# Kernel tuning notes

Hardware: AMD Instinct MI355X
Metric: run time of the kernel (lower is better)

The kernel has to match this reference:

```python
import jax, jax.numpy as jnp
import numpy as np
from jax import lax

B, T, F, H = 8192, 512, 24, 12


def setup_inputs() -> dict:
    key = jax.random.key(0)
    ks = jax.random.split(key, 12)
    s_in = 1.0 / np.sqrt(H)  # PyTorch RNN init scale: U(-1/sqrt(H), 1/sqrt(H))
    u = lambda k, shape, s: jax.random.uniform(k, shape, jnp.float32, -s, s)
    return {
        "x": jax.random.normal(ks[0], (B, T, F), jnp.float32),
        "W_ih": u(ks[1], (H, F), s_in),
        "b_ih": u(ks[2], (H,), s_in),
        "W_hh": u(ks[3], (H, H), s_in),
        "b_hh": u(ks[4], (H,), s_in),
        "W1": u(ks[5], (H, H), 1.0 / np.sqrt(H)),
        "b1": u(ks[6], (H,), 1.0 / np.sqrt(H)),
        "W2": u(ks[7], (H, H), 1.0 / np.sqrt(H)),
        "b2": u(ks[8], (H,), 1.0 / np.sqrt(H)),
        "W3": u(ks[9], (1, H), 1.0 / np.sqrt(H)),
        "b3": u(ks[10], (1,), 1.0 / np.sqrt(H)),
    }


def reference(x, W_ih, b_ih, W_hh, b_hh, W1, b1, W2, b2, W3, b3):
    # Precompute input projection for all timesteps: [B,T,H]
    xp = jnp.einsum("btf,hf->bth", x, W_ih) + b_ih

    def step(h, xt):  # h: [B,H], xt: [B,H]
        h = jnp.tanh(xt + h @ W_hh.T + b_hh)
        return h, None

    h0 = jnp.zeros((x.shape[0], W_hh.shape[0]), x.dtype)
    hT, _ = lax.scan(step, h0, jnp.swapaxes(xp, 0, 1))  # scan over time

    out = jax.nn.relu(hT @ W1.T + b1)
    out = jax.nn.relu(out @ W2.T + b2)
    out = (out @ W3.T + b3).reshape(-1)  # [B]
    return out
```

## Files before the change

### kernel.cpp

```cpp
#include <hip/hip_runtime.h>
#include <stdint.h>

#define BB 8192
#define TT 512
#define FF 24
#define HH 12

#define CHAINS 8
#define TC 16
#define CHUNKS (TT / TC)
#define CHUNK_BYTES (TC * FF * 4)
#define LDS_STRIDE (CHUNK_BYTES + 16)
#define NLOAD 13
#define BUF_BYTES (NLOAD * 1024)
#define X_CHAIN_BYTES (TT * FF * 4)

typedef const __attribute__((address_space(1))) void* gptr_t;
typedef __attribute__((address_space(3))) void* lptr_t;

__device__ __forceinline__ float fast_tanh(float x) {
  float e = __expf(x + x);
  float r = __builtin_amdgcn_rcpf(e + 1.0f);
  return fmaf(-2.0f, r, 1.0f);
}

__global__ __launch_bounds__(64, 1) void rnn_fused(
    const float* __restrict__ x, const float* __restrict__ W_ih,
    const float* __restrict__ b_ih, const float* __restrict__ W_hh,
    const float* __restrict__ b_hh, const float* __restrict__ W1,
    const float* __restrict__ b1, const float* __restrict__ W2,
    const float* __restrict__ b2, const float* __restrict__ W3,
    const float* __restrict__ b3, float* __restrict__ out) {
  __shared__ __align__(16) char smem[2 * BUF_BYTES];

  const int lane  = threadIdx.x;
  const int chain = lane >> 3;
  const int m     = lane & 3;
  const int sub   = (lane >> 2) & 1;

  float wih[3][12];
  float whh[3][12];
  float bcv[3];
  const int r0 = 3 * m;
#pragma unroll
  for (int r = 0; r < 3; ++r) {
    const float4* wr = (const float4*)(W_ih + (r0 + r) * FF + sub * 12);
    float4 a = wr[0], b = wr[1], c = wr[2];
    wih[r][0] = a.x; wih[r][1] = a.y; wih[r][2]  = a.z; wih[r][3]  = a.w;
    wih[r][4] = b.x; wih[r][5] = b.y; wih[r][6]  = b.z; wih[r][7]  = b.w;
    wih[r][8] = c.x; wih[r][9] = c.y; wih[r][10] = c.z; wih[r][11] = c.w;
    bcv[r] = b_ih[r0 + r] + b_hh[r0 + r];
#pragma unroll
    for (int k = 0; k < 12; ++k) {
      const int K = k / 3, cc = k % 3;
      const int col = 3 * (m ^ K) + cc;
      whh[r][k] = W_hh[(r0 + r) * HH + col];
    }
  }

  unsigned voff[NLOAD];
#pragma unroll
  for (int k = 0; k < NLOAD; ++k) {
    unsigned off = (unsigned)(k * 1024) + (unsigned)(lane * 16);
    unsigned c = off / LDS_STRIDE;
    unsigned w = off - c * LDS_STRIDE;
    bool ok = (c < CHAINS) && (w < CHUNK_BYTES);
    voff[k] = ok ? (c * X_CHAIN_BYTES + w) : 0u;
  }

  const char* xg = (const char*)x + (size_t)blockIdx.x * CHAINS * X_CHAIN_BYTES;

#pragma unroll
  for (int k = 0; k < NLOAD; ++k)
    __builtin_amdgcn_global_load_lds((gptr_t)(xg + voff[k]),
                                     (lptr_t)(smem + k * 1024), 16, 0, 0);

  float h[12];
#pragma unroll
  for (int k = 0; k < 12; ++k) h[k] = 0.0f;

  for (int ch = 0; ch < CHUNKS; ++ch) {
    if (ch + 1 < CHUNKS) {
      const char* gb = xg + (size_t)(ch + 1) * CHUNK_BYTES;
      char* lb = smem + ((ch + 1) & 1) * BUF_BYTES;
#pragma unroll
      for (int k = 0; k < NLOAD; ++k)
        __builtin_amdgcn_global_load_lds((gptr_t)(gb + voff[k]),
                                         (lptr_t)(lb + k * 1024), 16, 0, 0);
      asm volatile("s_waitcnt vmcnt(13)" ::: "memory");
    } else {
      asm volatile("s_waitcnt vmcnt(0)" ::: "memory");
    }

    const char* bufc = smem + (ch & 1) * BUF_BYTES + chain * LDS_STRIDE + sub * 48;
#pragma unroll
    for (int t = 0; t < TC; ++t) {
      const float4* xp = (const float4*)(bufc + t * 96);
      float4 x0 = xp[0], x1 = xp[1], x2 = xp[2];
      float xs[12] = {x0.x, x0.y, x0.z, x0.w, x1.x, x1.y,
                      x1.z, x1.w, x2.x, x2.y, x2.z, x2.w};
      float av[3];
#pragma unroll
      for (int r = 0; r < 3; ++r) {
        float pa = 0.0f, pb = 0.0f;
#pragma unroll
        for (int j = 0; j < 6; ++j) {
          pa = fmaf(wih[r][j], xs[j], pa);
          pb = fmaf(wih[r][j + 6], xs[j + 6], pb);
        }
        float p = pa + pb;
        p += __shfl_xor(p, 4);
        float ra = 0.0f, rb = 0.0f;
#pragma unroll
        for (int k = 0; k < 6; ++k) {
          ra = fmaf(whh[r][k], h[k], ra);
          rb = fmaf(whh[r][k + 6], h[k + 6], rb);
        }
        av[r] = fast_tanh(p + (ra + rb) + bcv[r]);
      }
      float bv[3], cv[3], dv[3];
#pragma unroll
      for (int r = 0; r < 3; ++r) bv[r] = __shfl_xor(av[r], 1);
#pragma unroll
      for (int r = 0; r < 3; ++r) {
        cv[r] = __shfl_xor(av[r], 2);
        dv[r] = __shfl_xor(bv[r], 2);
      }
#pragma unroll
      for (int r = 0; r < 3; ++r) {
        h[r] = av[r]; h[3 + r] = bv[r]; h[6 + r] = cv[r]; h[9 + r] = dv[r];
      }
    }
  }

  if ((lane & 7) == 0) {
    float o1[12], o2[12];
#pragma unroll
    for (int i = 0; i < 12; ++i) {
      float acc = b1[i];
#pragma unroll
      for (int j = 0; j < 12; ++j) acc = fmaf(W1[i * 12 + j], h[j], acc);
      o1[i] = fmaxf(acc, 0.0f);
    }
#pragma unroll
    for (int i = 0; i < 12; ++i) {
      float acc = b2[i];
#pragma unroll
      for (int j = 0; j < 12; ++j) acc = fmaf(W2[i * 12 + j], o1[j], acc);
      o2[i] = fmaxf(acc, 0.0f);
    }
    float o = b3[0];
#pragma unroll
    for (int j = 0; j < 12; ++j) o = fmaf(W3[j], o2[j], o);
    out[blockIdx.x * CHAINS + chain] = o;
  }
}

extern "C" void kernel_launch(void* const* d_in, const int* in_sizes, int n_in,
                              void* d_out, int out_size, void* d_ws, size_t ws_size,
                              hipStream_t stream) {
  (void)in_sizes; (void)n_in; (void)d_ws; (void)ws_size; (void)out_size;
  const float* x    = (const float*)d_in[0];
  const float* W_ih = (const float*)d_in[1];
  const float* b_ih = (const float*)d_in[2];
  const float* W_hh = (const float*)d_in[3];
  const float* b_hh = (const float*)d_in[4];
  const float* W1   = (const float*)d_in[5];
  const float* b1   = (const float*)d_in[6];
  const float* W2   = (const float*)d_in[7];
  const float* b2   = (const float*)d_in[8];
  const float* W3   = (const float*)d_in[9];
  const float* b3   = (const float*)d_in[10];

  rnn_fused<<<dim3(BB / CHAINS), dim3(64), 0, stream>>>(
      x, W_ih, b_ih, W_hh, b_hh, W1, b1, W2, b2, W3, b3, (float*)d_out);
}
```

Baseline: 597.4 us.

## Split RNN into producer waves for input projection and consumer wave for recurrence

The kernel is restructured into a producer/consumer block of 256 threads. Three waves compute the input projection for 64 chains into a double-buffered LDS area. One wave runs the recurrence with one batch chain per lane and the full W_hh held in registers, using packed FMAs and no cross-lane shuffles. The grid drops from 1024 one-wave blocks to 128 four-wave blocks, so fewer CUs are occupied, and only one serial wave per block does the recurrence, which risks lower overall parallelism.

```diff
diff --git a/kernel.cpp b/kernel.cpp
--- a/kernel.cpp
+++ b/kernel.cpp
@@ -6,17 +6,14 @@
 #define FF 24
 #define HH 12
 
-#define CHAINS 8
-#define TC 16
-#define CHUNKS (TT / TC)
-#define CHUNK_BYTES (TC * FF * 4)
-#define LDS_STRIDE (CHUNK_BYTES + 16)
-#define NLOAD 13
-#define BUF_BYTES (NLOAD * 1024)
-#define X_CHAIN_BYTES (TT * FF * 4)
+#define NCHAIN 64
+#define TC 8
+#define NCHUNK (TT / TC)
+#define ROWF 13
+#define CHSTRIDE (TC * ROWF + 1)
+#define BUFN (NCHAIN * CHSTRIDE)
 
-typedef const __attribute__((address_space(1))) void* gptr_t;
-typedef __attribute__((address_space(3))) void* lptr_t;
+typedef float v2f __attribute__((ext_vector_type(2)));
 
 __device__ __forceinline__ float fast_tanh(float x) {
   float e = __expf(x + x);
@@ -24,116 +21,109 @@
   return fmaf(-2.0f, r, 1.0f);
 }
 
-__global__ __launch_bounds__(64, 1) void rnn_fused(
+__global__ __launch_bounds__(256, 1) void rnn_pc(
     const float* __restrict__ x, const float* __restrict__ W_ih,
     const float* __restrict__ b_ih, const float* __restrict__ W_hh,
     const float* __restrict__ b_hh, const float* __restrict__ W1,
     const float* __restrict__ b1, const float* __restrict__ W2,
     const float* __restrict__ b2, const float* __restrict__ W3,
     const float* __restrict__ b3, float* __restrict__ out) {
-  __shared__ __align__(16) char smem[2 * BUF_BYTES];
+  __shared__ float xpb[2][BUFN];
 
-  const int lane  = threadIdx.x;
-  const int chain = lane >> 3;
-  const int m     = lane & 3;
-  const int sub   = (lane >> 2) & 1;
+  const int tid  = threadIdx.x;
+  const int wid  = tid >> 6;
+  const int lane = tid & 63;
+  const int bid  = blockIdx.x;
 
-  float wih[3][12];
-  float whh[3][12];
-  float bcv[3];
-  const int r0 = 3 * m;
+  if (wid < 3) {
+    const int jbase = wid * 4;
+    v2f wih[4][12];
+    float bs[4];
 #pragma unroll
-  for (int r = 0; r < 3; ++r) {
-    const float4* wr = (const float4*)(W_ih + (r0 + r) * FF + sub * 12);
-    float4 a = wr[0], b = wr[1], c = wr[2];
-    wih[r][0] = a.x; wih[r][1] = a.y; wih[r][2]  = a.z; wih[r][3]  = a.w;
-    wih[r][4] = b.x; wih[r][5] = b.y; wih[r][6]  = b.z; wih[r][7]  = b.w;
-    wih[r][8] = c.x; wih[r][9] = c.y; wih[r][10] = c.z; wih[r][11] = c.w;
-    bcv[r] = b_ih[r0 + r] + b_hh[r0 + r];
+    for (int r = 0; r < 4; ++r) {
+      bs[r] = b_ih[jbase + r] + b_hh[jbase + r];
 #pragma unroll
-    for (int k = 0; k < 12; ++k) {
-      const int K = k / 3, cc = k % 3;
-      const int col = 3 * (m ^ K) + cc;
-      whh[r][k] = W_hh[(r0 + r) * HH + col];
-    }
-  }
-
-  unsigned voff[NLOAD];
-#pragma unroll
-  for (int k = 0; k < NLOAD; ++k) {
-    unsigned off = (unsigned)(k * 1024) + (unsigned)(lane * 16);
-    unsigned c = off / LDS_STRIDE;
-    unsigned w = off - c * LDS_STRIDE;
-    bool ok = (c < CHAINS) && (w < CHUNK_BYTES);
-    voff[k] = ok ? (c * X_CHAIN_BYTES + w) : 0u;
-  }
-
-  const char* xg = (const char*)x + (size_t)blockIdx.x * CHAINS * X_CHAIN_BYTES;
-
-#pragma unroll
-  for (int k = 0; k < NLOAD; ++k)
-    __builtin_amdgcn_global_load_lds((gptr_t)(xg + voff[k]),
-                                     (lptr_t)(smem + k * 1024), 16, 0, 0);
-
-  float h[12];
-#pragma unroll
-  for (int k = 0; k < 12; ++k) h[k] = 0.0f;
-
-  for (int ch = 0; ch < CHUNKS; ++ch) {
-    if (ch + 1 < CHUNKS) {
-      const char* gb = xg + (size_t)(ch + 1) * CHUNK_BYTES;
-      char* lb = smem + ((ch + 1) & 1) * BUF_BYTES;
-#pragma unroll
-      for (int k = 0; k < NLOAD; ++k)
-        __builtin_amdgcn_global_load_lds((gptr_t)(gb + voff[k]),
-                                         (lptr_t)(lb + k * 1024), 16, 0, 0);
-      asm volatile("s_waitcnt vmcnt(13)" ::: "memory");
-    } else {
-      asm volatile("s_waitcnt vmcnt(0)" ::: "memory");
+      for (int k = 0; k < 12; ++k)
+        wih[r][k] = *(const v2f*)(W_ih + (jbase + r) * FF + 2 * k);
     }
 
-    const char* bufc = smem + (ch & 1) * BUF_BYTES + chain * LDS_STRIDE + sub * 48;
+    auto fill = [&](int cc) {
+      float* buf = &xpb[cc & 1][0];
+#pragma unroll 2
+      for (int i = 0; i < (NCHAIN * TC) / 64; ++i) {
+        const int p = i * 64 + lane;
+        const int chain = p >> 3;
+        const int t = p & (TC - 1);
+        const float4* xr =
+            (const float4*)(x + ((size_t)(bid * NCHAIN + chain) * TT +
+                                 (cc * TC + t)) * FF);
+        float4 a0 = xr[0], a1 = xr[1], a2 = xr[2];
+        float4 a3 = xr[3], a4 = xr[4], a5 = xr[5];
+        v2f xv[12] = {{a0.x, a0.y}, {a0.z, a0.w}, {a1.x, a1.y}, {a1.z, a1.w},
+                      {a2.x, a2.y}, {a2.z, a2.w}, {a3.x, a3.y}, {a3.z, a3.w},
+                      {a4.x, a4.y}, {a4.z, a4.w}, {a5.x, a5.y}, {a5.z, a5.w}};
+        float* dst = buf + chain * CHSTRIDE + t * ROWF + jbase;
 #pragma unroll
-    for (int t = 0; t < TC; ++t) {
-      const float4* xp = (const float4*)(bufc + t * 96);
-      float4 x0 = xp[0], x1 = xp[1], x2 = xp[2];
-      float xs[12] = {x0.x, x0.y, x0.z, x0.w, x1.x, x1.y,
-                      x1.z, x1.w, x2.x, x2.y, x2.z, x2.w};
-      float av[3];
+        for (int r = 0; r < 4; ++r) {
+          v2f s = {0.0f, 0.0f};
 #pragma unroll
-      for (int r = 0; r < 3; ++r) {
-        float pa = 0.0f, pb = 0.0f;
+          for (int k = 0; k < 12; ++k)
+            s = __builtin_elementwise_fma(wih[r][k], xv[k], s);
+          dst[r] = bs[r] + s.x + s.y;
+        }
+      }
+    };
+
+    fill(0);
+    for (int c = 0; c < NCHUNK; ++c) {
+      __syncthreads();
+      if (c + 1 < NCHUNK) fill(c + 1);
+    }
+  } else {
+    v2f whh[12][6];
 #pragma unroll
-        for (int j = 0; j < 6; ++j) {
-          pa = fmaf(wih[r][j], xs[j], pa);
-          pb = fmaf(wih[r][j + 6], xs[j + 6], pb);
+    for (int j = 0; j < 12; ++j)
+#pragma unroll
+      for (int k = 0; k < 6; ++k)
+        whh[j][k] = *(const v2f*)(W_hh + j * HH + 2 * k);
+
+    v2f hv[6];
+#pragma unroll
+    for (int k = 0; k < 6; ++k) hv[k] = (v2f){0.0f, 0.0f};
+
+    for (int c = 0; c < NCHUNK; ++c) {
+      __syncthreads();
+      const float* bufc = &xpb[c & 1][lane * CHSTRIDE];
+      float xc[12], xn[12];
+#pragma unroll
+      for (int j = 0; j < 12; ++j) xc[j] = bufc[j];
+#pragma unroll
+      for (int t = 0; t < TC; ++t) {
+        if (t + 1 < TC) {
+#pragma unroll
+          for (int j = 0; j < 12; ++j) xn[j] = bufc[(t + 1) * ROWF + j];
         }
-        float p = pa + pb;
-        p += __shfl_xor(p, 4);
-        float ra = 0.0f, rb = 0.0f;
+        float nh[12];
 #pragma unroll
-        for (int k = 0; k < 6; ++k) {
-          ra = fmaf(whh[r][k], h[k], ra);
-          rb = fmaf(whh[r][k + 6], h[k + 6], rb);
+        for (int j = 0; j < 12; ++j) {
+          v2f s = {0.0f, 0.0f};
+#pragma unroll
+          for (int k = 0; k < 6; ++k)
+            s = __builtin_elementwise_fma(whh[j][k], hv[k], s);
+          nh[j] = fast_tanh(xc[j] + s.x + s.y);
         }
-        av[r] = fast_tanh(p + (ra + rb) + bcv[r]);
-      }
-      float bv[3], cv[3], dv[3];
 #pragma unroll
-      for (int r = 0; r < 3; ++r) bv[r] = __shfl_xor(av[r], 1);
+        for (int k = 0; k < 6; ++k) hv[k] = (v2f){nh[2 * k], nh[2 * k + 1]};
+        if (t + 1 < TC) {
 #pragma unroll
-      for (int r = 0; r < 3; ++r) {
-        cv[r] = __shfl_xor(av[r], 2);
-        dv[r] = __shfl_xor(bv[r], 2);
-      }
-#pragma unroll
-      for (int r = 0; r < 3; ++r) {
-        h[r] = av[r]; h[3 + r] = bv[r]; h[6 + r] = cv[r]; h[9 + r] = dv[r];
+          for (int j = 0; j < 12; ++j) xc[j] = xn[j];
+        }
       }
     }
-  }
 
-  if ((lane & 7) == 0) {
+    float h[12];
+#pragma unroll
+    for (int k = 0; k < 6; ++k) { h[2 * k] = hv[k].x; h[2 * k + 1] = hv[k].y; }
     float o1[12], o2[12];
 #pragma unroll
     for (int i = 0; i < 12; ++i) {
@@ -152,7 +142,7 @@
     float o = b3[0];
 #pragma unroll
     for (int j = 0; j < 12; ++j) o = fmaf(W3[j], o2[j], o);
-    out[blockIdx.x * CHAINS + chain] = o;
+    out[bid * NCHAIN + lane] = o;
   }
 }
 
@@ -172,6 +162,6 @@
   const float* W3   = (const float*)d_in[9];
   const float* b3   = (const float*)d_in[10];
 
-  rnn_fused<<<dim3(BB / CHAINS), dim3(64), 0, stream>>>(
+  rnn_pc<<<dim3(BB / NCHAIN), dim3(256), 0, stream>>>(
       x, W_ih, b_ih, W_hh, b_hh, W1, b1, W2, b2, W3, b3, (float*)d_out);
 }
```

Result: slower. 1.063 ms (+77.9%).
